# Kernel optimization log

Measured on AMD Instinct MI355X. Metric: run time of the kernel, lower is better.

Reference implementation:

```python
import math
import jax, jax.numpy as jnp
import numpy as np

B, S, H, NH = 8, 1024, 1024, 16
HD = H // NH  # head dim = 64

def setup_inputs() -> dict:
    key = jax.random.key(0)
    ks = jax.random.split(key, 4)
    scale = 1.0 / math.sqrt(H)
    return {
        "hidden_state": jax.random.normal(ks[0], (B, S, H), jnp.float32),
        "attention_mask": jnp.ones((B, 1, S), jnp.float32),
        "Wq": jax.random.normal(ks[1], (H, H), jnp.float32) * scale,
        "bq": jnp.zeros((H,), jnp.float32),
        "Wk": jax.random.normal(ks[2], (H, H), jnp.float32) * scale,
        "bk": jnp.zeros((H,), jnp.float32),
        "Wv": jax.random.normal(ks[3], (H, H), jnp.float32) * scale,
        "bv": jnp.zeros((H,), jnp.float32),
    }

def _split_heads(x):
    # [B,S,H] -> [B,NH,S,HD]
    return x.reshape(B, S, NH, HD).transpose(0, 2, 1, 3)

def reference(hidden_state, attention_mask, Wq, bq, Wk, bk, Wv, bv):
    q = _split_heads(hidden_state @ Wq.T + bq)
    k = _split_heads(hidden_state @ Wk.T + bk)
    v = _split_heads(hidden_state @ Wv.T + bv)
    scores = jnp.einsum("bhqd,bhkd->bhqk", q, k) / math.sqrt(HD)
    # mask [B,1,S] -> additive bias [B,1,S,1], broadcast over heads and keys
    bias = (1.0 - attention_mask)[..., None] * -10000.0
    scores = scores + bias
    probs = jax.nn.softmax(scores, axis=-1)  # dropout prob = 0.0 (eval)
    ctx = jnp.einsum("bhqk,bhkd->bhqd", probs, v)
    return ctx.transpose(0, 2, 1, 3).reshape(B, S, H)
```

## Files before the change

kernel.cpp:

```cpp
#include <hip/hip_runtime.h>
#include <hip/hip_bf16.h>


typedef __attribute__((ext_vector_type(8))) short bf16x8;
typedef __attribute__((ext_vector_type(4))) float f32x4;
typedef unsigned short u16;

#define NB 8
#define NS 1024
#define NH_ 16
#define HD_ 64
#define QKV_T (NB * NH_ * NS * HD_)
#define XN (8192 * 1024)
#define WN (1024 * 1024)
#define QSCL 0.180336880f

static __device__ __forceinline__ u16 f2bf(float f) {
    unsigned int u = __float_as_uint(f);
    u += 0x7FFFu + ((u >> 16) & 1u);
    return (u16)(u >> 16);
}

static __device__ __forceinline__ bf16x8 cvt8(const float* p) {
    float4 a = *(const float4*)p;
    float4 b = *(const float4*)(p + 4);
    union { bf16x8 v; u16 s[8]; } r;
    r.s[0] = f2bf(a.x); r.s[1] = f2bf(a.y); r.s[2] = f2bf(a.z); r.s[3] = f2bf(a.w);
    r.s[4] = f2bf(b.x); r.s[5] = f2bf(b.y); r.s[6] = f2bf(b.z); r.s[7] = f2bf(b.w);
    return r.v;
}

static __device__ __forceinline__ void async16(const u16* g, u16* l) {
    __builtin_amdgcn_global_load_lds((const __attribute__((address_space(1))) void*)g,
                                     (__attribute__((address_space(3))) void*)l,
                                     16, 0, 0);
}

static __device__ __forceinline__ unsigned int cvtpk(float a, float b) {
    unsigned int r;
    asm("v_cvt_pk_bf16_f32 %0, %1, %2" : "=v"(r) : "v"(a), "v"(b));
    return r;
}

__global__ __launch_bounds__(256) void cvt_pass(
    const float* __restrict__ X,
    const float* __restrict__ Wq, const float* __restrict__ Wk,
    const float* __restrict__ Wv,
    u16* __restrict__ Xb, u16* __restrict__ Wb)
{
    size_t i8 = ((size_t)blockIdx.x * 256 + threadIdx.x) * 8;
    if (i8 < XN) {
        *(bf16x8*)(Xb + i8) = cvt8(X + i8);
    } else {
        size_t j = i8 - XN;
        int w = (int)(j >> 20);
        const float* src = (w == 0) ? Wq : (w == 1) ? Wk : Wv;
        *(bf16x8*)(Wb + j) = cvt8(src + (j & (WN - 1)));
    }
}

#define GEMM_LDS_BYTES (128 * 132 * 2)
__global__ __launch_bounds__(256) void qkv_gemm_bf16(
    const u16* __restrict__ Xb, const u16* __restrict__ Wb,
    const float* __restrict__ bq, const float* __restrict__ bk,
    const float* __restrict__ bv,
    u16* __restrict__ qkv)
{
    extern __shared__ u16 smem[];
    u16* As = smem;
    u16* Bs = smem + 128 * 64;
    u16* Cs = smem;

    const int tid  = threadIdx.x;
    const int lane = tid & 63;
    const int wid  = tid >> 6;
    const int l15  = lane & 15;
    const int quad = lane >> 4;
    const int sw   = l15 & 7;
    const int wm   = (wid >> 1) * 64;
    const int wn   = (wid & 1) * 64;

    const int bid = blockIdx.x;
    const int x   = bid & 7;
    const int j   = bid >> 3;
    const int m0  = (x * 8 + (j & 7)) * 128;
    const int nb  = (j >> 3) * 128;

    f32x4 acc[4][4];
#pragma unroll
    for (int mi = 0; mi < 4; ++mi)
#pragma unroll
        for (int ni = 0; ni < 4; ++ni) acc[mi][ni] = (f32x4){0.f, 0.f, 0.f, 0.f};

    for (int kt = 0; kt < 16; ++kt) {
#pragma unroll
        for (int it = 0; it < 4; ++it) {
            int idx = it * 256 + tid;
            int row = idx >> 3, kc = idx & 7;
            int kcs = (kc ^ (row & 7)) * 8;
            async16(Xb + (size_t)(m0 + row) * 1024 + kt * 64 + kcs, As + idx * 8);
            async16(Wb + (size_t)(nb + row) * 1024 + kt * 64 + kcs, Bs + idx * 8);
        }
        __syncthreads();
#pragma unroll
        for (int kk = 0; kk < 2; ++kk) {
            bf16x8 a[4], b[4];
#pragma unroll
            for (int mi = 0; mi < 4; ++mi)
                a[mi] = *(const bf16x8*)&As[(wm + mi * 16 + l15) * 64 + (((kk * 4 + quad) ^ sw) * 8)];
#pragma unroll
            for (int ni = 0; ni < 4; ++ni)
                b[ni] = *(const bf16x8*)&Bs[(wn + ni * 16 + l15) * 64 + (((kk * 4 + quad) ^ sw) * 8)];
#pragma unroll
            for (int mi = 0; mi < 4; ++mi)
#pragma unroll
                for (int ni = 0; ni < 4; ++ni)
                    acc[mi][ni] = __builtin_amdgcn_mfma_f32_16x16x32_bf16(
                        a[mi], b[ni], acc[mi][ni], 0, 0, 0);
        }
        __syncthreads();
    }

    const int which = nb >> 10;
    const int ncol0 = nb & 1023;
    const int batch = m0 >> 10;
    const float* bias = (which == 0) ? bq : (which == 1) ? bk : bv;
    const float scl   = (which == 0) ? QSCL : 1.0f;

    if (which == 2) {
#pragma unroll
        for (int ni = 0; ni < 4; ++ni) {
            int nn = ncol0 + wn + ni * 16 + l15;
            float bia = bias[nn];
            int h = nn >> 6;
            int d = nn & 63;
            size_t base = (size_t)((2 * NB + batch) * NH_ + h) * (NS * HD_);
#pragma unroll
            for (int mi = 0; mi < 4; ++mi) {
                int s_base = ((m0 + wm + mi * 16 + quad * 4) & 1023);
                ushort4 pk;
                pk.x = f2bf(acc[mi][ni][0] + bia);
                pk.y = f2bf(acc[mi][ni][1] + bia);
                pk.z = f2bf(acc[mi][ni][2] + bia);
                pk.w = f2bf(acc[mi][ni][3] + bia);
                *(ushort4*)&qkv[base + (size_t)d * NS + s_base] = pk;
            }
        }
    } else {
#pragma unroll
        for (int ni = 0; ni < 4; ++ni) {
            int col = wn + ni * 16 + l15;
            float bia = bias[ncol0 + col];
#pragma unroll
            for (int mi = 0; mi < 4; ++mi)
#pragma unroll
                for (int r = 0; r < 4; ++r)
                    Cs[(wm + mi * 16 + quad * 4 + r) * 132 + col] =
                        f2bf((acc[mi][ni][r] + bia) * scl);
        }
        __syncthreads();
        const size_t tb = (size_t)((which * NB + batch) * NH_) * (NS * HD_);
        const int h0 = ncol0 >> 6;
#pragma unroll
        for (int it = 0; it < 8; ++it) {
            int idx = it * 256 + tid;
            int row = idx >> 4;
            int c   = idx & 15;
            int h   = h0 + (c >> 3);
            int s   = (m0 + row) & 1023;
            *(uint4*)&qkv[tb + (size_t)h * (NS * HD_) + (size_t)s * HD_ + (c & 7) * 8] =
                *(const uint4*)&Cs[row * 132 + c * 8];
        }
    }
}

__global__ __launch_bounds__(256) void qkv_gemm_f32(
    const float* __restrict__ X,
    const float* __restrict__ Wq, const float* __restrict__ bq,
    const float* __restrict__ Wk, const float* __restrict__ bk,
    const float* __restrict__ Wv, const float* __restrict__ bv,
    u16* __restrict__ qkv)
{
    __shared__ u16 As[128 * 72];
    __shared__ u16 Bs[128 * 72];
    const int tid  = threadIdx.x;
    const int lane = tid & 63;
    const int wid  = tid >> 6;
    const int l15  = lane & 15;
    const int quad = lane >> 4;
    const int wm   = (wid >> 1) * 64;
    const int wn   = (wid & 1) * 64;
    const int m0   = blockIdx.x * 128;
    const int nb   = blockIdx.y * 128;
    const int which = nb >> 10;
    const int ncol0 = nb & 1023;
    const float* W    = (which == 0) ? Wq : (which == 1) ? Wk : Wv;
    const float* bias = (which == 0) ? bq : (which == 1) ? bk : bv;
    const float scl   = (which == 0) ? QSCL : 1.0f;

    f32x4 acc[4][4];
#pragma unroll
    for (int mi = 0; mi < 4; ++mi)
#pragma unroll
        for (int ni = 0; ni < 4; ++ni) acc[mi][ni] = (f32x4){0.f, 0.f, 0.f, 0.f};

    for (int kt = 0; kt < 16; ++kt) {
#pragma unroll
        for (int it = 0; it < 4; ++it) {
            int idx = it * 256 + tid;
            int row = idx >> 3, c = idx & 7;
            *(bf16x8*)&As[row * 72 + c * 8] = cvt8(&X[(size_t)(m0 + row) * 1024 + kt * 64 + c * 8]);
            *(bf16x8*)&Bs[row * 72 + c * 8] = cvt8(&W[(size_t)(ncol0 + row) * 1024 + kt * 64 + c * 8]);
        }
        __syncthreads();
#pragma unroll
        for (int kk = 0; kk < 2; ++kk) {
            bf16x8 a[4], b[4];
#pragma unroll
            for (int mi = 0; mi < 4; ++mi)
                a[mi] = *(const bf16x8*)&As[(wm + mi * 16 + l15) * 72 + kk * 32 + quad * 8];
#pragma unroll
            for (int ni = 0; ni < 4; ++ni)
                b[ni] = *(const bf16x8*)&Bs[(wn + ni * 16 + l15) * 72 + kk * 32 + quad * 8];
#pragma unroll
            for (int mi = 0; mi < 4; ++mi)
#pragma unroll
                for (int ni = 0; ni < 4; ++ni)
                    acc[mi][ni] = __builtin_amdgcn_mfma_f32_16x16x32_bf16(
                        a[mi], b[ni], acc[mi][ni], 0, 0, 0);
        }
        __syncthreads();
    }
#pragma unroll
    for (int ni = 0; ni < 4; ++ni) {
        int nn = ncol0 + wn + ni * 16 + l15;
        float bia = bias[nn];
        int h = nn >> 6;
        int d = nn & 63;
#pragma unroll
        for (int mi = 0; mi < 4; ++mi) {
#pragma unroll
            for (int r = 0; r < 4; ++r) {
                int rg    = m0 + wm + mi * 16 + quad * 4 + r;
                int batch = rg >> 10;
                int s     = rg & 1023;
                size_t base = (size_t)((which * NB + batch) * NH_ + h) * (NS * HD_);
                size_t off  = (which == 2) ? base + (size_t)d * NS + s
                                           : base + (size_t)s * HD_ + d;
                qkv[off] = f2bf((acc[mi][ni][r] + bia) * scl);
            }
        }
    }
}

__global__ __launch_bounds__(256) void attn(
    const u16* __restrict__ qkv, float* __restrict__ out)
{
    __shared__ u16 Ks[2][64 * 64];
    __shared__ u16 VTs[2][64 * 64];
    __shared__ u16 Ps[128 * 72];

    const int tid  = threadIdx.x;
    const int lane = tid & 63;
    const int wid  = tid >> 6;
    const int l15  = lane & 15;
    const int quad = lane >> 4;
    const int sw   = l15 & 7;

    const int id    = blockIdx.x;
    const int hb    = (id & 7) * 16 + ((id >> 3) >> 3);
    const int q0    = ((id >> 3) & 7) * 128;
    const int h     = hb & 15;
    const int batch = hb >> 4;

    const size_t headoff = (size_t)(batch * NH_ + h) * (NS * HD_);
    const u16* Qg = qkv + headoff;
    const u16* Kg = qkv + (size_t)QKV_T + headoff;
    const u16* Vt = qkv + (size_t)2 * QKV_T + headoff;

    const u16* kp[2];
    const u16* vp[2];
#pragma unroll
    for (int it = 0; it < 2; ++it) {
        int idx = it * 256 + tid;
        int row = idx >> 3, kc = idx & 7;
        int kcs = (kc ^ (row & 7)) * 8;
        kp[it] = Kg + (size_t)row * 64 + kcs;
        vp[it] = Vt + (size_t)row * NS + kcs;
    }

    bf16x8 aq[2][2];
#pragma unroll
    for (int f = 0; f < 2; ++f)
#pragma unroll
        for (int kk = 0; kk < 2; ++kk)
            aq[f][kk] = *(const bf16x8*)&Qg[(size_t)(q0 + wid * 32 + f * 16 + l15) * 64 + kk * 32 + quad * 8];

#pragma unroll
    for (int it = 0; it < 2; ++it) {
        int idx = it * 256 + tid;
        async16(kp[it], Ks[0] + idx * 8);
        async16(vp[it], VTs[0] + idx * 8);
    }
    __syncthreads();

    float lsum[2] = {0.f, 0.f};
    f32x4 o[2][4];
#pragma unroll
    for (int f = 0; f < 2; ++f)
#pragma unroll
        for (int ni = 0; ni < 4; ++ni) o[f][ni] = (f32x4){0.f, 0.f, 0.f, 0.f};

    for (int kt = 0; kt < 16; ++kt) {
        const u16* Kc = Ks[kt & 1];
        const u16* Vc = VTs[kt & 1];

        if (kt < 15) {
            u16* Kn = Ks[(kt & 1) ^ 1];
            u16* Vn = VTs[(kt & 1) ^ 1];
#pragma unroll
            for (int it = 0; it < 2; ++it) {
                int idx = it * 256 + tid;
                async16(kp[it] + (size_t)(kt + 1) * 4096, Kn + idx * 8);
                async16(vp[it] + (size_t)(kt + 1) * 64, Vn + idx * 8);
            }
        }

        f32x4 sfr[2][4];
        __builtin_amdgcn_s_setprio(1);
#pragma unroll
        for (int ni = 0; ni < 4; ++ni) {
            bf16x8 b0 = *(const bf16x8*)&Kc[(ni * 16 + l15) * 64 + ((quad ^ sw) * 8)];
            bf16x8 b1 = *(const bf16x8*)&Kc[(ni * 16 + l15) * 64 + (((4 + quad) ^ sw) * 8)];
#pragma unroll
            for (int f = 0; f < 2; ++f) {
                f32x4 sa = (f32x4){0.f, 0.f, 0.f, 0.f};
                sa = __builtin_amdgcn_mfma_f32_16x16x32_bf16(b0, aq[f][0], sa, 0, 0, 0);
                sa = __builtin_amdgcn_mfma_f32_16x16x32_bf16(b1, aq[f][1], sa, 0, 0, 0);
                sfr[f][ni] = sa;
            }
        }
        __builtin_amdgcn_s_setprio(0);

#pragma unroll
        for (int f = 0; f < 2; ++f)
#pragma unroll
            for (int ni = 0; ni < 4; ++ni) {
                float p0 = __builtin_amdgcn_exp2f(sfr[f][ni][0]);
                float p1 = __builtin_amdgcn_exp2f(sfr[f][ni][1]);
                float p2 = __builtin_amdgcn_exp2f(sfr[f][ni][2]);
                float p3 = __builtin_amdgcn_exp2f(sfr[f][ni][3]);
                lsum[f] += (p0 + p1) + (p2 + p3);
                uint2 pk;
                pk.x = cvtpk(p0, p1);
                pk.y = cvtpk(p2, p3);
                *(uint2*)&Ps[(wid * 32 + f * 16 + l15) * 72 + ni * 16 + quad * 4] = pk;
            }

        __builtin_amdgcn_s_setprio(1);
#pragma unroll
        for (int kk = 0; kk < 2; ++kk) {
            bf16x8 ap[2];
#pragma unroll
            for (int f = 0; f < 2; ++f)
                ap[f] = *(const bf16x8*)&Ps[(wid * 32 + f * 16 + l15) * 72 + kk * 32 + quad * 8];
#pragma unroll
            for (int ni = 0; ni < 4; ++ni) {
                bf16x8 bv_ = *(const bf16x8*)&Vc[(ni * 16 + l15) * 64 + (((kk * 4 + quad) ^ sw) * 8)];
#pragma unroll
                for (int f = 0; f < 2; ++f)
                    o[f][ni] = __builtin_amdgcn_mfma_f32_16x16x32_bf16(ap[f], bv_, o[f][ni], 0, 0, 0);
            }
        }
        __builtin_amdgcn_s_setprio(0);
        __syncthreads();
    }

#pragma unroll
    for (int f = 0; f < 2; ++f) {
        lsum[f] += __shfl_xor(lsum[f], 16, 64);
        lsum[f] += __shfl_xor(lsum[f], 32, 64);
    }

#pragma unroll
    for (int f = 0; f < 2; ++f) {
        float inv[4];
#pragma unroll
        for (int r = 0; r < 4; ++r)
            inv[r] = 1.0f / __shfl(lsum[f], quad * 4 + r, 64);
#pragma unroll
        for (int ni = 0; ni < 4; ++ni)
#pragma unroll
            for (int r = 0; r < 4; ++r) {
                int row = wid * 32 + f * 16 + quad * 4 + r;
                out[(size_t)(batch * NS + q0 + row) * 1024 + h * 64 + ni * 16 + l15] =
                    o[f][ni][r] * inv[r];
            }
    }
}

extern "C" void kernel_launch(void* const* d_in, const int* in_sizes, int n_in,
                              void* d_out, int out_size, void* d_ws, size_t ws_size,
                              hipStream_t stream) {
    const float* X  = (const float*)d_in[0];
    const float* Wq = (const float*)d_in[2];
    const float* bq = (const float*)d_in[3];
    const float* Wk = (const float*)d_in[4];
    const float* bk = (const float*)d_in[5];
    const float* Wv = (const float*)d_in[6];
    const float* bv = (const float*)d_in[7];
    float* outp = (float*)d_out;

    u16* qkv = (u16*)d_ws;
    u16* Xb  = (u16*)((char*)d_ws + (size_t)QKV_T * 3 * 2);
    u16* Wb  = Xb + XN;
    const size_t need = (size_t)QKV_T * 3 * 2 + (size_t)XN * 2 + (size_t)3 * WN * 2;

    if (ws_size >= need) {
        cvt_pass<<<(XN + 3 * WN) / 8 / 256, 256, 0, stream>>>(X, Wq, Wk, Wv, Xb, Wb);
        qkv_gemm_bf16<<<1536, 256, GEMM_LDS_BYTES, stream>>>(Xb, Wb, bq, bk, bv, qkv);
    } else {
        qkv_gemm_f32<<<dim3(64, 24), 256, 0, stream>>>(X, Wq, bq, Wk, bk, Wv, bv, qkv);
    }
    attn<<<1024, 256, 0, stream>>>(qkv, outp);
}
```

Baseline: 217.9 us.

## Replace QKV GEMM with 256x256-tile double-buffered 8-phase pipelined kernel

The 128x128 single-buffered bf16 GEMM is replaced by a 512-thread kernel that computes a 256x256 tile. It uses 128KB of LDS split into two buffers, each holding A and B halves. Async global-to-LDS loads for the next K slices are interleaved with MFMA work in eight phases, using explicit vmcnt waits, raw barriers and s_setprio around the MFMA bursts. The aim is to hide load latency behind compute and raise data reuse per tile, at the cost of large LDS use (one block per CU), high register pressure and a fragile hand-written synchronisation schedule.

Result: no change. 221.3 us (+1.5%).

```diff
diff --git a/kernel.cpp b/kernel.cpp
--- a/kernel.cpp
+++ b/kernel.cpp
@@ -59,17 +59,15 @@
     }
 }
 
-#define GEMM_LDS_BYTES (128 * 132 * 2)
-__global__ __launch_bounds__(256) void qkv_gemm_bf16(
+#define GEMM2_LDS_BYTES 131072
+
+__global__ __launch_bounds__(512, 2) void qkv_gemm_8ph(
     const u16* __restrict__ Xb, const u16* __restrict__ Wb,
     const float* __restrict__ bq, const float* __restrict__ bk,
     const float* __restrict__ bv,
     u16* __restrict__ qkv)
 {
-    extern __shared__ u16 smem[];
-    u16* As = smem;
-    u16* Bs = smem + 128 * 64;
-    u16* Cs = smem;
+    extern __shared__ u16 sm[];
 
     const int tid  = threadIdx.x;
     const int lane = tid & 63;
@@ -77,101 +75,163 @@
     const int l15  = lane & 15;
     const int quad = lane >> 4;
     const int sw   = l15 & 7;
-    const int wm   = (wid >> 1) * 64;
-    const int wn   = (wid & 1) * 64;
+    const int wr   = wid >> 2;
+    const int wc   = wid & 3;
 
     const int bid = blockIdx.x;
-    const int x   = bid & 7;
-    const int j   = bid >> 3;
-    const int m0  = (x * 8 + (j & 7)) * 128;
-    const int nb  = (j >> 3) * 128;
-
-    f32x4 acc[4][4];
-#pragma unroll
-    for (int mi = 0; mi < 4; ++mi)
-#pragma unroll
-        for (int ni = 0; ni < 4; ++ni) acc[mi][ni] = (f32x4){0.f, 0.f, 0.f, 0.f};
-
-    for (int kt = 0; kt < 16; ++kt) {
-#pragma unroll
-        for (int it = 0; it < 4; ++it) {
-            int idx = it * 256 + tid;
-            int row = idx >> 3, kc = idx & 7;
-            int kcs = (kc ^ (row & 7)) * 8;
-            async16(Xb + (size_t)(m0 + row) * 1024 + kt * 64 + kcs, As + idx * 8);
-            async16(Wb + (size_t)(nb + row) * 1024 + kt * 64 + kcs, Bs + idx * 8);
-        }
-        __syncthreads();
-#pragma unroll
-        for (int kk = 0; kk < 2; ++kk) {
-            bf16x8 a[4], b[4];
+    const int wg  = (bid & 7) * 48 + (bid >> 3);
+    const int m0  = (wg & 31) * 256;
+    const int n0  = (wg >> 5) * 256;
+
+    const u16* Ap = Xb + (size_t)m0 * 1024;
+    const u16* Bp = Wb + (size_t)n0 * 1024;
+
+    int offG[2], offL[2];
+#pragma unroll
+    for (int it = 0; it < 2; ++it) {
+        int idx = it * 512 + tid;
+        int lr = idx >> 3, kc = idx & 7;
+        offG[it] = lr * 1024 + ((kc ^ (lr & 7)) * 8);
+        offL[it] = idx * 8;
+    }
+
+    const int arow = wr * 64 + l15;
+    const int brow = wc * 32 + l15;
+
+    f32x4 acc[2][2][4][2];
+#pragma unroll
+    for (int qm = 0; qm < 2; ++qm)
+#pragma unroll
+        for (int qn = 0; qn < 2; ++qn)
 #pragma unroll
             for (int mi = 0; mi < 4; ++mi)
-                a[mi] = *(const bf16x8*)&As[(wm + mi * 16 + l15) * 64 + (((kk * 4 + quad) ^ sw) * 8)];
-#pragma unroll
-            for (int ni = 0; ni < 4; ++ni)
-                b[ni] = *(const bf16x8*)&Bs[(wn + ni * 16 + l15) * 64 + (((kk * 4 + quad) ^ sw) * 8)];
-#pragma unroll
-            for (int mi = 0; mi < 4; ++mi)
-#pragma unroll
-                for (int ni = 0; ni < 4; ++ni)
-                    acc[mi][ni] = __builtin_amdgcn_mfma_f32_16x16x32_bf16(
-                        a[mi], b[ni], acc[mi][ni], 0, 0, 0);
-        }
-        __syncthreads();
-    }
-
-    const int which = nb >> 10;
-    const int ncol0 = nb & 1023;
+#pragma unroll
+                for (int ni = 0; ni < 2; ++ni)
+                    acc[qm][qn][mi][ni] = (f32x4){0.f, 0.f, 0.f, 0.f};
+
+    bf16x8 a[4][2], b[2][2];
+
+#define STG_A(BUF, H, T) do { if ((T) < 16) { \
+    _Pragma("unroll") for (int it = 0; it < 2; ++it) \
+        async16(Ap + (size_t)(H) * 131072 + (T) * 64 + offG[it], \
+                sm + ((BUF) * 4 + (H)) * 8192 + offL[it]); } } while (0)
+#define STG_B(BUF, H, T) do { if ((T) < 16) { \
+    _Pragma("unroll") for (int it = 0; it < 2; ++it) \
+        async16(Bp + (size_t)(H) * 131072 + (T) * 64 + offG[it], \
+                sm + ((BUF) * 4 + 2 + (H)) * 8192 + offL[it]); } } while (0)
+#define LDA(BUF, QM) do { \
+    _Pragma("unroll") for (int mi = 0; mi < 4; ++mi) { \
+        _Pragma("unroll") for (int kk = 0; kk < 2; ++kk) \
+            a[mi][kk] = *(const bf16x8*)&sm[((BUF) * 4 + (QM)) * 8192 + \
+                (arow + mi * 16) * 64 + (((kk * 4 + quad) ^ sw) * 8)]; } } while (0)
+#define LDB(BUF, QN) do { \
+    _Pragma("unroll") for (int ni = 0; ni < 2; ++ni) { \
+        _Pragma("unroll") for (int kk = 0; kk < 2; ++kk) \
+            b[ni][kk] = *(const bf16x8*)&sm[((BUF) * 4 + 2 + (QN)) * 8192 + \
+                (brow + ni * 16) * 64 + (((kk * 4 + quad) ^ sw) * 8)]; } } while (0)
+#define MM(QM, QN) do { __builtin_amdgcn_s_setprio(1); \
+    _Pragma("unroll") for (int kk = 0; kk < 2; ++kk) \
+    _Pragma("unroll") for (int mi = 0; mi < 4; ++mi) \
+    _Pragma("unroll") for (int ni = 0; ni < 2; ++ni) \
+        acc[QM][QN][mi][ni] = __builtin_amdgcn_mfma_f32_16x16x32_bf16( \
+            a[mi][kk], b[ni][kk], acc[QM][QN][mi][ni], 0, 0, 0); \
+    __builtin_amdgcn_s_setprio(0); } while (0)
+#define BAR asm volatile("s_barrier" ::: "memory")
+#define WAITV4 asm volatile("s_waitcnt vmcnt(4)" ::: "memory")
+#define WAITV0 asm volatile("s_waitcnt vmcnt(0)" ::: "memory")
+
+    STG_A(0, 0, 0); STG_B(0, 1, 0); STG_A(0, 1, 0);
+    STG_B(0, 0, 0); STG_A(1, 0, 1); STG_B(1, 1, 1);
+    WAITV4;
+    BAR;
+
+    for (int jj = 0; jj < 8; ++jj) {
+        const int j0 = jj * 2, j1 = j0 + 1;
+        LDA(0, 0); LDB(0, 0); STG_A(1, 1, j0 + 1); MM(0, 0); BAR;
+        LDB(0, 1);            STG_B(1, 0, j0 + 1); MM(0, 1); BAR;
+        LDA(0, 1);            STG_A(0, 0, j0 + 2); MM(1, 1); BAR;
+        LDB(0, 0);            STG_B(0, 1, j0 + 2); MM(1, 0);
+        if (jj == 7) { WAITV0; } else { WAITV4; }
+        BAR;
+        LDA(1, 0); LDB(1, 0); STG_A(0, 1, j1 + 1); MM(0, 0); BAR;
+        LDB(1, 1);            STG_B(0, 0, j1 + 1); MM(0, 1); BAR;
+        LDA(1, 1);            STG_A(1, 0, j1 + 2); MM(1, 1); BAR;
+        LDB(1, 0);            STG_B(1, 1, j1 + 2); MM(1, 0);
+        if (jj < 7) { WAITV4; BAR; }
+    }
+
+    const int which = n0 >> 10;
+    const int ncol0 = n0 & 1023;
     const int batch = m0 >> 10;
+    const int mrow0 = m0 & 1023;
     const float* bias = (which == 0) ? bq : (which == 1) ? bk : bv;
     const float scl   = (which == 0) ? QSCL : 1.0f;
 
     if (which == 2) {
 #pragma unroll
-        for (int ni = 0; ni < 4; ++ni) {
-            int nn = ncol0 + wn + ni * 16 + l15;
-            float bia = bias[nn];
-            int h = nn >> 6;
-            int d = nn & 63;
-            size_t base = (size_t)((2 * NB + batch) * NH_ + h) * (NS * HD_);
-#pragma unroll
-            for (int mi = 0; mi < 4; ++mi) {
-                int s_base = ((m0 + wm + mi * 16 + quad * 4) & 1023);
-                ushort4 pk;
-                pk.x = f2bf(acc[mi][ni][0] + bia);
-                pk.y = f2bf(acc[mi][ni][1] + bia);
-                pk.z = f2bf(acc[mi][ni][2] + bia);
-                pk.w = f2bf(acc[mi][ni][3] + bia);
-                *(ushort4*)&qkv[base + (size_t)d * NS + s_base] = pk;
-            }
-        }
+        for (int qm = 0; qm < 2; ++qm)
+#pragma unroll
+            for (int qn = 0; qn < 2; ++qn)
+#pragma unroll
+                for (int ni = 0; ni < 2; ++ni) {
+                    int col = ncol0 + qn * 128 + wc * 32 + ni * 16 + l15;
+                    float bia = bias[col];
+                    int h = col >> 6;
+                    int d = col & 63;
+                    size_t base = (size_t)((2 * NB + batch) * NH_ + h) * (NS * HD_);
+#pragma unroll
+                    for (int mi = 0; mi < 4; ++mi) {
+                        int s = mrow0 + qm * 128 + wr * 64 + mi * 16 + quad * 4;
+                        ushort4 pk;
+                        pk.x = f2bf(acc[qm][qn][mi][ni][0] + bia);
+                        pk.y = f2bf(acc[qm][qn][mi][ni][1] + bia);
+                        pk.z = f2bf(acc[qm][qn][mi][ni][2] + bia);
+                        pk.w = f2bf(acc[qm][qn][mi][ni][3] + bia);
+                        *(ushort4*)&qkv[base + (size_t)d * NS + s] = pk;
+                    }
+                }
     } else {
-#pragma unroll
-        for (int ni = 0; ni < 4; ++ni) {
-            int col = wn + ni * 16 + l15;
-            float bia = bias[ncol0 + col];
-#pragma unroll
-            for (int mi = 0; mi < 4; ++mi)
-#pragma unroll
-                for (int r = 0; r < 4; ++r)
-                    Cs[(wm + mi * 16 + quad * 4 + r) * 132 + col] =
-                        f2bf((acc[mi][ni][r] + bia) * scl);
-        }
-        __syncthreads();
+        u16* Cs = sm;
         const size_t tb = (size_t)((which * NB + batch) * NH_) * (NS * HD_);
         const int h0 = ncol0 >> 6;
-#pragma unroll
-        for (int it = 0; it < 8; ++it) {
-            int idx = it * 256 + tid;
-            int row = idx >> 4;
-            int c   = idx & 15;
-            int h   = h0 + (c >> 3);
-            int s   = (m0 + row) & 1023;
-            *(uint4*)&qkv[tb + (size_t)h * (NS * HD_) + (size_t)s * HD_ + (c & 7) * 8] =
-                *(const uint4*)&Cs[row * 132 + c * 8];
-        }
-    }
+        __syncthreads();
+#pragma unroll
+        for (int qm = 0; qm < 2; ++qm) {
+            if (qm) __syncthreads();
+#pragma unroll
+            for (int qn = 0; qn < 2; ++qn)
+#pragma unroll
+                for (int ni = 0; ni < 2; ++ni) {
+                    int col = qn * 128 + wc * 32 + ni * 16 + l15;
+                    float bia = bias[ncol0 + col];
+#pragma unroll
+                    for (int mi = 0; mi < 4; ++mi)
+#pragma unroll
+                        for (int r = 0; r < 4; ++r)
+                            Cs[(wr * 64 + mi * 16 + quad * 4 + r) * 264 + col] =
+                                f2bf((acc[qm][qn][mi][ni][r] + bia) * scl);
+                }
+            __syncthreads();
+#pragma unroll
+            for (int it = 0; it < 8; ++it) {
+                int idx = it * 512 + tid;
+                int lr = idx >> 5;
+                int c  = idx & 31;
+                int s  = mrow0 + qm * 128 + lr;
+                int h  = h0 + (c >> 3);
+                *(uint4*)&qkv[tb + (size_t)h * (NS * HD_) + (size_t)s * HD_ + (c & 7) * 8] =
+                    *(const uint4*)&Cs[lr * 264 + c * 8];
+            }
+        }
+    }
+#undef STG_A
+#undef STG_B
+#undef LDA
+#undef LDB
+#undef MM
+#undef BAR
+#undef WAITV4
+#undef WAITV0
 }
 
 __global__ __launch_bounds__(256) void qkv_gemm_f32(
@@ -416,9 +476,17 @@
     u16* Wb  = Xb + XN;
     const size_t need = (size_t)QKV_T * 3 * 2 + (size_t)XN * 2 + (size_t)3 * WN * 2;
 
+    static bool attr_done = false;
+    if (!attr_done) {
+        (void)hipFuncSetAttribute((const void*)qkv_gemm_8ph,
+                                  hipFuncAttributeMaxDynamicSharedMemorySize,
+                                  GEMM2_LDS_BYTES);
+        attr_done = true;
+    }
+
     if (ws_size >= need) {
         cvt_pass<<<(XN + 3 * WN) / 8 / 256, 256, 0, stream>>>(X, Wq, Wk, Wv, Xb, Wb);
-        qkv_gemm_bf16<<<1536, 256, GEMM_LDS_BYTES, stream>>>(Xb, Wb, bq, bk, bv, qkv);
+        qkv_gemm_8ph<<<384, 512, GEMM2_LDS_BYTES, stream>>>(Xb, Wb, bq, bk, bv, qkv);
     } else {
         qkv_gemm_f32<<<dim3(64, 24), 256, 0, stream>>>(X, Wq, bq, Wk, bk, Wv, bv, qkv);
     }
```
